# Performance work log

Measured on AMD Instinct MI355X. Metric: run time of the kernel, lower is better.

The kernel has to match this reference:

```python
import jax, jax.numpy as jnp
import numpy as np

V, H, L, T, B, S = 32000, 1024, 2, 64, 32, 64


def setup_inputs() -> dict:
    key = jax.random.key(0)
    ks = jax.random.split(key, 10)
    sc = 0.02
    return {
        "tokens": jax.random.randint(ks[0], (T, B), 0, V),
        "h0": jax.random.normal(ks[1], (L, B, H), jnp.float32) * sc,
        "c0": jax.random.normal(ks[2], (L, B, H), jnp.float32) * sc,
        "contexts": jax.random.normal(ks[3], (B, S, H), jnp.float32) * sc,
        "emb": jax.random.normal(ks[4], (V, H), jnp.float32) * sc,
        "W_ih": jax.random.normal(ks[5], (L, 4 * H, H), jnp.float32) * sc,
        "W_hh": jax.random.normal(ks[6], (L, 4 * H, H), jnp.float32) * sc,
        "b_ih": jnp.zeros((L, 4 * H), jnp.float32),
        "b_hh": jnp.zeros((L, 4 * H), jnp.float32),
        "W_in": jax.random.normal(ks[7], (H, H), jnp.float32) * sc,
        "b_in": jnp.zeros((H,), jnp.float32),
        "W_out": jax.random.normal(ks[8], (H, 2 * H), jnp.float32) * sc,
        "b_out": jnp.zeros((H,), jnp.float32),
    }


def _lstm_cell(x, h, c, Wih, Whh, bih, bhh):
    # PyTorch LSTMCell gate order: i, f, g, o
    gates = x @ Wih.T + bih + h @ Whh.T + bhh  # [B, 4H]
    i, f, g, o = jnp.split(gates, 4, axis=-1)
    c1 = jax.nn.sigmoid(f) * c + jax.nn.sigmoid(i) * jnp.tanh(g)
    h1 = jax.nn.sigmoid(o) * jnp.tanh(c1)
    return h1, c1


def reference(tokens, h0, c0, contexts, emb, W_ih, W_hh, b_ih, b_hh,
              W_in, b_in, W_out, b_out):
    # dropout is identity in eval mode
    embs = emb[tokens]  # [T, B, H]
    n_layers = h0.shape[0]

    def step(carry, x):
        h, c = carry
        hs, cs = [], []
        inp = x
        for l in range(n_layers):
            h1, c1 = _lstm_cell(inp, h[l], c[l], W_ih[l], W_hh[l], b_ih[l], b_hh[l])
            inp = h1
            hs.append(h1)
            cs.append(c1)
        # global (Luong general) attention
        gamma = inp @ W_in.T + b_in                      # [B, H]
        scores = jnp.einsum("bsh,bh->bs", contexts, gamma)
        w = jax.nn.softmax(scores, axis=-1)              # [B, S]
        ctx = jnp.einsum("bs,bsh->bh", w, contexts)      # [B, H]
        out = jnp.tanh(jnp.concatenate([ctx, inp], axis=-1) @ W_out.T + b_out)
        return (jnp.stack(hs), jnp.stack(cs)), (out, w)

    (hT, cT), (outputs, attns) = jax.lax.scan(step, (h0, c0), embs)
    return outputs, hT, cT  # outputs: [T, B, H]
```

## Files before the change

kernel.cpp:

```cpp
#include <hip/hip_runtime.h>
#include <hip/hip_bf16.h>

#define HDIM 1024
#define BDIM 32
#define TDIM 64
#define SDIM 64
#define NBLK 256

typedef __attribute__((ext_vector_type(8))) short short8;
typedef __attribute__((ext_vector_type(4))) short s4v;
typedef __attribute__((ext_vector_type(4))) float f32x4;
typedef unsigned short ushort;
typedef unsigned int uint;

__device__ __forceinline__ float sigm(float x){ return 1.f/(1.f+expf(-x)); }
__device__ __forceinline__ ushort f2bf(float x){
  uint u = __float_as_uint(x);
  u = (u + 0x7FFF + ((u>>16)&1)) >> 16;
  return (ushort)u;
}
#define MFMA16(a,b,c) __builtin_amdgcn_mfma_f32_16x16x32_bf16((a),(b),(c),0,0,0)
#define ALD(p)     __hip_atomic_load((p), __ATOMIC_RELAXED, __HIP_MEMORY_SCOPE_AGENT)
#define AST(p,v)   __hip_atomic_store((p),(v), __ATOMIC_RELAXED, __HIP_MEMORY_SCOPE_AGENT)


__global__ void init_state_kernel(const float* __restrict__ h0,
                                  ushort* __restrict__ h0h,
                                  ushort* __restrict__ h1h){
  int i = blockIdx.x*256 + threadIdx.x;
  int l = i >> 15, r = i & 32767;
  int b = r >> 10, h = r & 1023;
  ushort* dst = l ? h1h : h0h;
  dst[(h>>2)*128 + b*4 + (h&3)] = f2bf(h0[i]);
}

__global__ void bar_init_kernel(int* flags){
  for(int i=threadIdx.x; i<1024; i+=256) flags[i] = 0;
}

__global__ void cast_kernel(const float* __restrict__ src, ushort* __restrict__ dst, int n4){
  int i = blockIdx.x*256 + threadIdx.x;
  if(i < n4){
    float4 v = ((const float4*)src)[i];
    ushort4 o; o.x=f2bf(v.x); o.y=f2bf(v.y); o.z=f2bf(v.z); o.w=f2bf(v.w);
    ((ushort4*)dst)[i] = o;
  }
}

__global__ void transpose_ctx_kernel(const float* __restrict__ ctx, ushort* __restrict__ ctxT){
  int b = blockIdx.y;
  int n = blockIdx.x*64 + (threadIdx.x & 63);
  int s0 = (threadIdx.x >> 6) * 16;
  for(int s=s0; s<s0+16; s++){
    float v = ctx[((size_t)b*SDIM + s)*HDIM + n];
    ctxT[((size_t)b*HDIM + n)*SDIM + s] = f2bf(v);
  }
}

__global__ void bias_kernel(const float* __restrict__ b_ih, const float* __restrict__ b_hh,
                            float* __restrict__ bias0, float* __restrict__ bias1){
  int i = blockIdx.x*256 + threadIdx.x;
  bias0[i] = b_ih[i] + b_hh[i];
  bias1[i] = b_ih[4096+i] + b_hh[4096+i];
}

__global__ void embed_kernel(const int* __restrict__ tokens,
                             const float* __restrict__ emb,
                             ushort* __restrict__ Xb){
  int tb = blockIdx.x;
  int tok = tokens[tb];
  const float4* src = (const float4*)(emb + (size_t)tok*HDIM);
  ushort4* dst = (ushort4*)(Xb + (size_t)tb*HDIM);
  float4 v = src[threadIdx.x];
  ushort4 o; o.x=f2bf(v.x); o.y=f2bf(v.y); o.z=f2bf(v.z); o.w=f2bf(v.w);
  dst[threadIdx.x] = o;
}

__global__ __launch_bounds__(256) void gemm_mfma_bt(
    const ushort* __restrict__ A0, const ushort* __restrict__ A1, int lda, int KSPLIT,
    const ushort* __restrict__ B, int ldb,
    const float* __restrict__ bias,
    float* __restrict__ C, int ldc, int K, int act){
  __shared__ ushort As[64][40];
  __shared__ ushort Bs[64][40];
  const int bm = blockIdx.y*64, bn = blockIdx.x*64;
  const int tid = threadIdx.x, w = tid>>6, lane = tid&63;
  const int quad = lane>>4, l16 = lane&15;
  const int mh = (w>>1)*32, nh = (w&1)*32;
  const int arow = tid>>2, aseg = (tid&3)*8;
  f32x4 acc[2][2];
  #pragma unroll
  for(int i=0;i<2;i++)
    #pragma unroll
    for(int j=0;j<2;j++) acc[i][j] = (f32x4){0.f,0.f,0.f,0.f};

  for(int k0=0;k0<K;k0+=32){
    int gk = k0 + aseg;
    const ushort* ap = (gk < KSPLIT) ? (A0 + (size_t)(bm+arow)*lda + gk)
                                     : (A1 + (size_t)(bm+arow)*lda + (gk - KSPLIT));
    *(float4*)&As[arow][aseg] = *(const float4*)ap;
    *(float4*)&Bs[arow][aseg] = *(const float4*)(B + (size_t)(bn+arow)*ldb + k0 + aseg);
    __syncthreads();
    short8 a0 = *(const short8*)&As[mh + l16][quad*8];
    short8 a1 = *(const short8*)&As[mh + 16 + l16][quad*8];
    short8 b0 = *(const short8*)&Bs[nh + l16][quad*8];
    short8 b1 = *(const short8*)&Bs[nh + 16 + l16][quad*8];
    acc[0][0] = MFMA16(a0, b0, acc[0][0]);
    acc[0][1] = MFMA16(a0, b1, acc[0][1]);
    acc[1][0] = MFMA16(a1, b0, acc[1][0]);
    acc[1][1] = MFMA16(a1, b1, acc[1][1]);
    __syncthreads();
  }
  #pragma unroll
  for(int mi=0;mi<2;mi++){
    #pragma unroll
    for(int r=0;r<4;r++){
      int row = bm + mh + mi*16 + quad*4 + r;
      #pragma unroll
      for(int ni=0;ni<2;ni++){
        int col = bn + nh + ni*16 + l16;
        float v = acc[mi][ni][r];
        if(bias) v += bias[col];
        if(act==1) v = tanhf(v);
        if(act==2) ((ushort*)C)[(size_t)row*ldc + col] = f2bf(v);
        else       C[(size_t)row*ldc + col] = v;
      }
    }
  }
}

__global__ __launch_bounds__(256,1) void lstm_skew(
    const ushort* __restrict__ Whh0b,
    const ushort* __restrict__ Wih1b,
    const ushort* __restrict__ Whh1b,
    const float*  __restrict__ G0,
    const float*  __restrict__ bias1c,
    const float*  __restrict__ c0in,
    ushort* __restrict__ h0h,
    ushort* __restrict__ h1h,
    ushort* __restrict__ inp_bf,
    float*  __restrict__ outstate,
    int* __restrict__ flags){
  extern __shared__ char smem[];
  ushort (*W0s)[1032]   = (ushort(*)[1032])smem;
  ushort (*W1s)[2056]   = (ushort(*)[2056])(smem + 33024);
  float (*gred0)[32][17] = (float(*)[32][17])(smem + 98816);
  float (*gred1)[32][17] = (float(*)[32][17])(smem + 107520);
  float (*cloc0)[4]      = (float(*)[4])(smem + 116224);
  float (*cloc1)[4]      = (float(*)[4])(smem + 116736);

  const int tid = threadIdx.x, w = tid>>6, lane = tid&63;
  const int quad = lane>>4, l16 = lane&15;
  const int blk = blockIdx.x;
  const int j0 = blk*4;

  {
    int r = tid>>4, seg = tid&15;
    int wr = (r>>2)*1024 + j0 + (r&3);
    const ushort* s0 = Whh0b + (size_t)wr*1024 + seg*64;
    const ushort* s1 = Wih1b + (size_t)wr*1024 + seg*64;
    const ushort* s2 = Whh1b + (size_t)wr*1024 + seg*64;
    #pragma unroll
    for(int u=0; u<64; u+=8){
      *(short8*)&W0s[r][seg*64+u]       = *(const short8*)(s0+u);
      *(short8*)&W1s[r][seg*64+u]       = *(const short8*)(s1+u);
      *(short8*)&W1s[r][1024+seg*64+u]  = *(const short8*)(s2+u);
    }
  }
  if(tid < 128){
    int b = tid>>2, jj = tid&3;
    cloc0[b][jj] = c0in[b*1024 + j0 + jj];
    cloc1[b][jj] = c0in[32768 + b*1024 + j0 + jj];
  }
  float2 pbI={0,0}, pbF={0,0}, pbG={0,0}, pbO={0,0};
  if(tid >= 64 && tid < 128){
    const float* br = bias1c + j0 + ((tid-64)&1)*2;
    pbI = *(const float2*)(br);
    pbF = *(const float2*)(br+1024);
    pbG = *(const float2*)(br+2048);
    pbO = *(const float2*)(br+3072);
  }
  __syncthreads();

  for(int p=0; p<=TDIM; p++){
    const ushort* h0p = h0h + (size_t)p*32768;
    ushort*       h0n = h0h + (size_t)(p+1)*32768;
    const ushort* h1m = h1h + (size_t)(p>0?p-1:0)*32768;
    ushort*       h1c = h1h + (size_t)p*32768;
    float2 pgI={0,0}, pgF={0,0}, pgG={0,0}, pgO={0,0};
    if(p < TDIM && tid < 64){
      const float* g0r = G0 + (size_t)(p*32+(tid>>1))*4096 + j0 + (tid&1)*2;
      pgI = *(const float2*)(g0r);
      pgF = *(const float2*)(g0r+1024);
      pgG = *(const float2*)(g0r+2048);
      pgO = *(const float2*)(g0r+3072);
    }
    if(p < TDIM){
      f32x4 acc0 = {0,0,0,0}, acc1 = {0,0,0,0};
      const int kbase = w*256;
      #pragma unroll
      for(int kc=0;kc<8;kc++){
        int k0 = kbase + kc*32 + quad*8;
        const ushort* pa = h0p + (k0>>2)*128 + l16*4;
        s4v a0lo = *(const s4v*)pa;
        s4v a0hi = *(const s4v*)(pa + 128);
        s4v a1lo = *(const s4v*)(pa + 64);
        s4v a1hi = *(const s4v*)(pa + 192);
        short8 af0 = __builtin_shufflevector(a0lo, a0hi, 0,1,2,3,4,5,6,7);
        short8 af1 = __builtin_shufflevector(a1lo, a1hi, 0,1,2,3,4,5,6,7);
        short8 bfrag = *(const short8*)&W0s[l16][k0];
        acc0 = MFMA16(af0, bfrag, acc0);
        acc1 = MFMA16(af1, bfrag, acc1);
      }
      #pragma unroll
      for(int r=0;r<4;r++){
        gred0[w][quad*4+r][l16]    = acc0[r];
        gred0[w][16+quad*4+r][l16] = acc1[r];
      }
    }
    if(p > 0){
      f32x4 acc0 = {0,0,0,0}, acc1 = {0,0,0,0};
      const ushort* hb1 = (w < 2) ? h0p : h1m;
      const int kb = (w&1)*512;
      #pragma unroll
      for(int kc=0;kc<16;kc++){
        int k0 = kb + kc*32 + quad*8;
        const ushort* pa = hb1 + (k0>>2)*128 + l16*4;
        s4v a0lo = *(const s4v*)pa;
        s4v a0hi = *(const s4v*)(pa + 128);
        s4v a1lo = *(const s4v*)(pa + 64);
        s4v a1hi = *(const s4v*)(pa + 192);
        short8 af0 = __builtin_shufflevector(a0lo, a0hi, 0,1,2,3,4,5,6,7);
        short8 af1 = __builtin_shufflevector(a1lo, a1hi, 0,1,2,3,4,5,6,7);
        short8 bfrag = *(const short8*)&W1s[l16][w*512 + kc*32 + quad*8];
        acc0 = MFMA16(af0, bfrag, acc0);
        acc1 = MFMA16(af1, bfrag, acc1);
      }
      #pragma unroll
      for(int r=0;r<4;r++){
        gred1[w][quad*4+r][l16]    = acc0[r];
        gred1[w][16+quad*4+r][l16] = acc1[r];
      }
    }
    __syncthreads();
    if(p < TDIM && tid < 64){
      int b = tid>>1, j2 = (tid&1)*2;
      ushort hv[2];
      #pragma unroll
      for(int u=0;u<2;u++){
        int jj = j2+u;
        float gi = u ? pgI.y : pgI.x;
        float gf = u ? pgF.y : pgF.x;
        float gg = u ? pgG.y : pgG.x;
        float go = u ? pgO.y : pgO.x;
        #pragma unroll
        for(int ww=0;ww<4;ww++){
          gi += gred0[ww][b][jj];    gf += gred0[ww][b][4+jj];
          gg += gred0[ww][b][8+jj];  go += gred0[ww][b][12+jj];
        }
        float c = cloc0[b][jj];
        float c1 = sigm(gf)*c + sigm(gi)*tanhf(gg);
        float h1 = sigm(go)*tanhf(c1);
        cloc0[b][jj] = c1;
        hv[u] = f2bf(h1);
        if(p==TDIM-1){
          outstate[b*1024 + j0 + jj] = h1;
          outstate[65536 + b*1024 + j0 + jj] = c1;
        }
      }
      uint pk = (uint)hv[0] | ((uint)hv[1] << 16);
      AST((uint*)(h0n + blk*128 + b*4 + j2), pk);
    }
    if(p > 0 && tid >= 64 && tid < 128){
      int ct = tid-64;
      int b = ct>>1, j2 = (ct&1)*2;
      ushort hv[2];
      #pragma unroll
      for(int u=0;u<2;u++){
        int jj = j2+u;
        float gi = u ? pbI.y : pbI.x;
        float gf = u ? pbF.y : pbF.x;
        float gg = u ? pbG.y : pbG.x;
        float go = u ? pbO.y : pbO.x;
        #pragma unroll
        for(int ww=0;ww<4;ww++){
          gi += gred1[ww][b][jj];    gf += gred1[ww][b][4+jj];
          gg += gred1[ww][b][8+jj];  go += gred1[ww][b][12+jj];
        }
        float c = cloc1[b][jj];
        float c1 = sigm(gf)*c + sigm(gi)*tanhf(gg);
        float h1 = sigm(go)*tanhf(c1);
        cloc1[b][jj] = c1;
        hv[u] = f2bf(h1);
        inp_bf[(size_t)((p-1)*32+b)*1024 + j0 + jj] = hv[u];
        if(p==TDIM){
          outstate[32768 + b*1024 + j0 + jj] = h1;
          outstate[98304 + b*1024 + j0 + jj] = c1;
        }
      }
      uint pk = (uint)hv[0] | ((uint)hv[1] << 16);
      AST((uint*)(h1c + blk*128 + b*4 + j2), pk);
    }
    if(p == TDIM) break;
    __syncthreads();
    const int target = p+1;
    if(tid==0) AST(&flags[blk], target);
    if(blk==0 && tid<64){
      while(true){
        int v0 = ALD(&flags[tid]);
        int v1 = ALD(&flags[tid+64]);
        int v2 = ALD(&flags[tid+128]);
        int v3 = ALD(&flags[tid+192]);
        int mn = min(min(v0,v1),min(v2,v3));
        if(__all(mn >= target)) break;
        __builtin_amdgcn_s_sleep(2);
      }
      if(tid<16) AST(&flags[512 + tid*32], target);
    }
    if(tid==0){
      while(ALD(&flags[512 + (blk>>4)*32]) < target) __builtin_amdgcn_s_sleep(8);
    }
    __syncthreads();
  }
}

__global__ __launch_bounds__(256) void attn_mfma(
    const ushort* __restrict__ gamma_bf,
    const ushort* __restrict__ ctxb,
    const ushort* __restrict__ ctxT,
    ushort* __restrict__ ctx_out){
  const int b = blockIdx.y, t0 = blockIdx.x*16;
  const int tid = threadIdx.x, w = tid>>6, lane = tid&63;
  const int quad = lane>>4, l16 = lane&15;
  __shared__ float S[16][68];
  __shared__ ushort Pb[16][72];
  {
    f32x4 acc = {0,0,0,0};
    const ushort* arow = gamma_bf + ((size_t)(t0+l16)*32 + b)*1024;
    const ushort* brow = ctxb + ((size_t)b*SDIM + w*16 + l16)*1024;
    #pragma unroll 8
    for(int kc=0;kc<32;kc++){
      short8 af = *(const short8*)(arow + kc*32 + quad*8);
      short8 bf = *(const short8*)(brow + kc*32 + quad*8);
      acc = MFMA16(af, bf, acc);
    }
    #pragma unroll
    for(int r=0;r<4;r++) S[quad*4+r][w*16+l16] = acc[r];
  }
  __syncthreads();
  if(tid < 16){
    float mx = -1e30f;
    for(int s=0;s<SDIM;s++) mx = fmaxf(mx, S[tid][s]);
    float sum = 0.f;
    for(int s=0;s<SDIM;s++) sum += expf(S[tid][s]-mx);
    float inv = 1.f/sum;
    for(int s=0;s<SDIM;s++) Pb[tid][s] = f2bf(expf(S[tid][s]-mx)*inv);
  }
  __syncthreads();
  const ushort* bbase = ctxT + ((size_t)b*HDIM + w*256)*SDIM;
  for(int nt=0; nt<16; nt++){
    f32x4 acc = {0,0,0,0};
    #pragma unroll
    for(int kc=0;kc<2;kc++){
      short8 af = *(const short8*)&Pb[l16][kc*32 + quad*8];
      short8 bf = *(const short8*)(bbase + (size_t)(nt*16+l16)*SDIM + kc*32 + quad*8);
      acc = MFMA16(af, bf, acc);
    }
    int n = w*256 + nt*16 + l16;
    #pragma unroll
    for(int r=0;r<4;r++){
      int t = t0 + quad*4 + r;
      ctx_out[((size_t)t*32 + b)*1024 + n] = f2bf(acc[r]);
    }
  }
}

extern "C" void kernel_launch(void* const* d_in, const int* in_sizes, int n_in,
                              void* d_out, int out_size, void* d_ws, size_t ws_size,
                              hipStream_t stream){
  const int*   tokens   = (const int*)  d_in[0];
  const float* h0       = (const float*)d_in[1];
  const float* c0       = (const float*)d_in[2];
  const float* contexts = (const float*)d_in[3];
  const float* emb      = (const float*)d_in[4];
  const float* W_ih     = (const float*)d_in[5];
  const float* W_hh     = (const float*)d_in[6];
  const float* b_ih     = (const float*)d_in[7];
  const float* b_hh     = (const float*)d_in[8];
  const float* W_in     = (const float*)d_in[9];
  const float* b_in     = (const float*)d_in[10];
  const float* W_out    = (const float*)d_in[11];
  const float* b_out    = (const float*)d_in[12];

  float* out = (float*)d_out;
  const int TB = TDIM*BDIM;

  char* wp = (char*)d_ws;
  float* G0      = (float*)wp;  wp += (size_t)TB*4*HDIM*4;
  float* bias0c  = (float*)wp;  wp += 4096*4;
  float* bias1c  = (float*)wp;  wp += 4096*4;
  int*   flags   = (int*)wp;    wp += 4096;
  ushort* X_bf   = (ushort*)wp; wp += (size_t)TB*HDIM*2;
  ushort* Wih0b  = (ushort*)wp; wp += (size_t)4*HDIM*HDIM*2;
  ushort* Whh0b  = (ushort*)wp; wp += (size_t)4*HDIM*HDIM*2;
  ushort* Wih1b  = (ushort*)wp; wp += (size_t)4*HDIM*HDIM*2;
  ushort* Whh1b  = (ushort*)wp; wp += (size_t)4*HDIM*HDIM*2;
  ushort* Winb   = (ushort*)wp; wp += (size_t)HDIM*HDIM*2;
  ushort* Woutb  = (ushort*)wp; wp += (size_t)HDIM*2*HDIM*2;
  ushort* inp_bf = (ushort*)wp; wp += (size_t)TB*HDIM*2;
  ushort* h0hist = (ushort*)wp; wp += (size_t)(TDIM+1)*BDIM*HDIM*2;
  ushort* h1hist = (ushort*)wp; wp += (size_t)(TDIM+1)*BDIM*HDIM*2;
  ushort* ctxb_bf= (ushort*)wp; wp += (size_t)BDIM*SDIM*HDIM*2;
  ushort* ctxT_bf= (ushort*)wp; wp += (size_t)BDIM*SDIM*HDIM*2;
  ushort* gammaB = (ushort*)G0;
  ushort* ctx_bf = X_bf;

  init_state_kernel<<<256,256,0,stream>>>(h0, h0hist, h1hist);
  bar_init_kernel<<<1,256,0,stream>>>(flags);
  cast_kernel<<<4096,256,0,stream>>>(W_ih,                       Wih0b, 4*HDIM*HDIM/4);
  cast_kernel<<<4096,256,0,stream>>>(W_hh,                       Whh0b, 4*HDIM*HDIM/4);
  cast_kernel<<<4096,256,0,stream>>>(W_ih + (size_t)4*HDIM*HDIM, Wih1b, 4*HDIM*HDIM/4);
  cast_kernel<<<4096,256,0,stream>>>(W_hh + (size_t)4*HDIM*HDIM, Whh1b, 4*HDIM*HDIM/4);
  cast_kernel<<<1024,256,0,stream>>>(W_in,  Winb,  HDIM*HDIM/4);
  cast_kernel<<<2048,256,0,stream>>>(W_out, Woutb, HDIM*2*HDIM/4);
  cast_kernel<<<2048,256,0,stream>>>(contexts, ctxb_bf, BDIM*SDIM*HDIM/4);
  transpose_ctx_kernel<<<dim3(16,32),256,0,stream>>>(contexts, ctxT_bf);
  bias_kernel<<<16,256,0,stream>>>(b_ih, b_hh, bias0c, bias1c);
  embed_kernel<<<TB,256,0,stream>>>(tokens, emb, X_bf);

  gemm_mfma_bt<<<dim3(4*HDIM/64, TB/64),256,0,stream>>>(
      X_bf, X_bf, HDIM, HDIM, Wih0b, HDIM, bias0c, G0, 4*HDIM, HDIM, 0);

  lstm_skew<<<NBLK,256,117248,stream>>>(
      Whh0b, Wih1b, Whh1b, G0, bias1c, c0,
      h0hist, h1hist, inp_bf, out + (size_t)TB*HDIM, flags);

  gemm_mfma_bt<<<dim3(HDIM/64, TB/64),256,0,stream>>>(
      inp_bf, inp_bf, HDIM, HDIM, Winb, HDIM, b_in, (float*)gammaB, HDIM, HDIM, 2);

  attn_mfma<<<dim3(4,32),256,0,stream>>>(gammaB, ctxb_bf, ctxT_bf, ctx_bf);

  gemm_mfma_bt<<<dim3(HDIM/64, TB/64),256,0,stream>>>(
      ctx_bf, inp_bf, HDIM, HDIM, Woutb, 2*HDIM, b_out, out, HDIM, 2*HDIM, 1);
}
```

Measured before the change: 930.2 us.

## Batch hidden-state loads upfront and slim grid barrier with double-buffered reductions

Issues all hidden-state fragment loads for both layers up front with inline-asm dwordx2 loads and one waitcnt, so the loads no longer sit between MFMAs. Double-buffers the gred reduction buffers by step parity, which removes the pre-barrier __syncthreads. The grid barrier now has per-wave flags written by the two writer waves after their stores drain, and every thread polls the release flag, which drops the trailing __syncthreads. This adds register pressure (96 s4v per thread) and a larger LDS footprint, and it relies on memory ordering held by relaxed atomics plus waitcnt.

```diff
diff --git a/kernel.cpp b/kernel.cpp
--- a/kernel.cpp
+++ b/kernel.cpp
@@ -22,6 +22,21 @@
 #define MFMA16(a,b,c) __builtin_amdgcn_mfma_f32_16x16x32_bf16((a),(b),(c),0,0,0)
 #define ALD(p)     __hip_atomic_load((p), __ATOMIC_RELAXED, __HIP_MEMORY_SCOPE_AGENT)
 #define AST(p,v)   __hip_atomic_store((p),(v), __ATOMIC_RELAXED, __HIP_MEMORY_SCOPE_AGENT)
+
+__device__ __forceinline__ void load8(const char* b, s4v* r){
+  asm volatile(
+    "global_load_dwordx2 %0, %8, off\n\t"
+    "global_load_dwordx2 %1, %8, off offset:128\n\t"
+    "global_load_dwordx2 %2, %8, off offset:256\n\t"
+    "global_load_dwordx2 %3, %8, off offset:384\n\t"
+    "global_load_dwordx2 %4, %8, off offset:2048\n\t"
+    "global_load_dwordx2 %5, %8, off offset:2176\n\t"
+    "global_load_dwordx2 %6, %8, off offset:2304\n\t"
+    "global_load_dwordx2 %7, %8, off offset:2432\n\t"
+    : "=&v"(r[0]), "=&v"(r[1]), "=&v"(r[2]), "=&v"(r[3]),
+      "=&v"(r[4]), "=&v"(r[5]), "=&v"(r[6]), "=&v"(r[7])
+    : "v"(b) : "memory");
+}
 
 
 __global__ void init_state_kernel(const float* __restrict__ h0,
@@ -144,10 +159,11 @@
   extern __shared__ char smem[];
   ushort (*W0s)[1032]   = (ushort(*)[1032])smem;
   ushort (*W1s)[2056]   = (ushort(*)[2056])(smem + 33024);
-  float (*gred0)[32][17] = (float(*)[32][17])(smem + 98816);
-  float (*gred1)[32][17] = (float(*)[32][17])(smem + 107520);
-  float (*cloc0)[4]      = (float(*)[4])(smem + 116224);
-  float (*cloc1)[4]      = (float(*)[4])(smem + 116736);
+  typedef float gredT[4][32][17];
+  gredT* gred0 = (gredT*)(smem + 98816);
+  gredT* gred1 = (gredT*)(smem + 116224);
+  float (*cloc0)[4]      = (float(*)[4])(smem + 133632);
+  float (*cloc1)[4]      = (float(*)[4])(smem + 134144);
 
   const int tid = threadIdx.x, w = tid>>6, lane = tid&63;
   const int quad = lane>>4, l16 = lane&15;
@@ -183,10 +199,12 @@
   __syncthreads();
 
   for(int p=0; p<=TDIM; p++){
+    const int par = p&1;
     const ushort* h0p = h0h + (size_t)p*32768;
     ushort*       h0n = h0h + (size_t)(p+1)*32768;
     const ushort* h1m = h1h + (size_t)(p>0?p-1:0)*32768;
     ushort*       h1c = h1h + (size_t)p*32768;
+
     float2 pgI={0,0}, pgF={0,0}, pgG={0,0}, pgO={0,0};
     if(p < TDIM && tid < 64){
       const float* g0r = G0 + (size_t)(p*32+(tid>>1))*4096 + j0 + (tid&1)*2;
@@ -195,51 +213,53 @@
       pgG = *(const float2*)(g0r+2048);
       pgO = *(const float2*)(g0r+3072);
     }
+
+    s4v r0[32]; s4v r1[64];
+    if(p < TDIM){
+      const char* b0 = (const char*)h0p + w*16384 + quad*512 + l16*8;
+      load8(b0,        r0);
+      load8(b0+4096,   r0+8);
+      load8(b0+8192,   r0+16);
+      load8(b0+12288,  r0+24);
+    }
+    if(p > 0){
+      const char* b1 = (const char*)((w<2)?h0p:h1m) + (w&1)*32768 + quad*512 + l16*8;
+      #pragma unroll
+      for(int i=0;i<8;i++) load8(b1 + i*4096, r1 + i*8);
+    }
+    asm volatile("s_waitcnt vmcnt(0)" ::: "memory");
+    __builtin_amdgcn_sched_barrier(0);
+
     if(p < TDIM){
       f32x4 acc0 = {0,0,0,0}, acc1 = {0,0,0,0};
-      const int kbase = w*256;
       #pragma unroll
       for(int kc=0;kc<8;kc++){
-        int k0 = kbase + kc*32 + quad*8;
-        const ushort* pa = h0p + (k0>>2)*128 + l16*4;
-        s4v a0lo = *(const s4v*)pa;
-        s4v a0hi = *(const s4v*)(pa + 128);
-        s4v a1lo = *(const s4v*)(pa + 64);
-        s4v a1hi = *(const s4v*)(pa + 192);
-        short8 af0 = __builtin_shufflevector(a0lo, a0hi, 0,1,2,3,4,5,6,7);
-        short8 af1 = __builtin_shufflevector(a1lo, a1hi, 0,1,2,3,4,5,6,7);
-        short8 bfrag = *(const short8*)&W0s[l16][k0];
+        short8 af0 = __builtin_shufflevector(r0[kc*4+0], r0[kc*4+2], 0,1,2,3,4,5,6,7);
+        short8 af1 = __builtin_shufflevector(r0[kc*4+1], r0[kc*4+3], 0,1,2,3,4,5,6,7);
+        short8 bfrag = *(const short8*)&W0s[l16][w*256 + kc*32 + quad*8];
         acc0 = MFMA16(af0, bfrag, acc0);
         acc1 = MFMA16(af1, bfrag, acc1);
       }
       #pragma unroll
       for(int r=0;r<4;r++){
-        gred0[w][quad*4+r][l16]    = acc0[r];
-        gred0[w][16+quad*4+r][l16] = acc1[r];
+        gred0[par][w][quad*4+r][l16]    = acc0[r];
+        gred0[par][w][16+quad*4+r][l16] = acc1[r];
       }
     }
     if(p > 0){
       f32x4 acc0 = {0,0,0,0}, acc1 = {0,0,0,0};
-      const ushort* hb1 = (w < 2) ? h0p : h1m;
-      const int kb = (w&1)*512;
       #pragma unroll
       for(int kc=0;kc<16;kc++){
-        int k0 = kb + kc*32 + quad*8;
-        const ushort* pa = hb1 + (k0>>2)*128 + l16*4;
-        s4v a0lo = *(const s4v*)pa;
-        s4v a0hi = *(const s4v*)(pa + 128);
-        s4v a1lo = *(const s4v*)(pa + 64);
-        s4v a1hi = *(const s4v*)(pa + 192);
-        short8 af0 = __builtin_shufflevector(a0lo, a0hi, 0,1,2,3,4,5,6,7);
-        short8 af1 = __builtin_shufflevector(a1lo, a1hi, 0,1,2,3,4,5,6,7);
+        short8 af0 = __builtin_shufflevector(r1[kc*4+0], r1[kc*4+2], 0,1,2,3,4,5,6,7);
+        short8 af1 = __builtin_shufflevector(r1[kc*4+1], r1[kc*4+3], 0,1,2,3,4,5,6,7);
         short8 bfrag = *(const short8*)&W1s[l16][w*512 + kc*32 + quad*8];
         acc0 = MFMA16(af0, bfrag, acc0);
         acc1 = MFMA16(af1, bfrag, acc1);
       }
       #pragma unroll
       for(int r=0;r<4;r++){
-        gred1[w][quad*4+r][l16]    = acc0[r];
-        gred1[w][16+quad*4+r][l16] = acc1[r];
+        gred1[par][w][quad*4+r][l16]    = acc0[r];
+        gred1[par][w][16+quad*4+r][l16] = acc1[r];
       }
     }
     __syncthreads();
@@ -255,8 +275,8 @@
         float go = u ? pgO.y : pgO.x;
         #pragma unroll
         for(int ww=0;ww<4;ww++){
-          gi += gred0[ww][b][jj];    gf += gred0[ww][b][4+jj];
-          gg += gred0[ww][b][8+jj];  go += gred0[ww][b][12+jj];
+          gi += gred0[par][ww][b][jj];    gf += gred0[par][ww][b][4+jj];
+          gg += gred0[par][ww][b][8+jj];  go += gred0[par][ww][b][12+jj];
         }
         float c = cloc0[b][jj];
         float c1 = sigm(gf)*c + sigm(gi)*tanhf(gg);
@@ -284,8 +304,8 @@
         float go = u ? pbO.y : pbO.x;
         #pragma unroll
         for(int ww=0;ww<4;ww++){
-          gi += gred1[ww][b][jj];    gf += gred1[ww][b][4+jj];
-          gg += gred1[ww][b][8+jj];  go += gred1[ww][b][12+jj];
+          gi += gred1[par][ww][b][jj];    gf += gred1[par][ww][b][4+jj];
+          gg += gred1[par][ww][b][8+jj];  go += gred1[par][ww][b][12+jj];
         }
         float c = cloc1[b][jj];
         float c1 = sigm(gf)*c + sigm(gi)*tanhf(gg);
@@ -302,25 +322,23 @@
       AST((uint*)(h1c + blk*128 + b*4 + j2), pk);
     }
     if(p == TDIM) break;
-    __syncthreads();
+
     const int target = p+1;
-    if(tid==0) AST(&flags[blk], target);
-    if(blk==0 && tid<64){
+    if(tid < 128){
+      asm volatile("s_waitcnt vmcnt(0)" ::: "memory");
+      if((tid&63)==0) AST(&flags[blk*2 + w], target);
+    }
+    if(blk==0 && tid < 64){
       while(true){
-        int v0 = ALD(&flags[tid]);
-        int v1 = ALD(&flags[tid+64]);
-        int v2 = ALD(&flags[tid+128]);
-        int v3 = ALD(&flags[tid+192]);
-        int mn = min(min(v0,v1),min(v2,v3));
+        int mn = 0x7fffffff;
+        #pragma unroll
+        for(int q=0;q<8;q++){ int v = ALD(&flags[tid + q*64]); mn = min(mn, v); }
         if(__all(mn >= target)) break;
-        __builtin_amdgcn_s_sleep(2);
-      }
-      if(tid<16) AST(&flags[512 + tid*32], target);
-    }
-    if(tid==0){
-      while(ALD(&flags[512 + (blk>>4)*32]) < target) __builtin_amdgcn_s_sleep(8);
-    }
-    __syncthreads();
+        __builtin_amdgcn_s_sleep(1);
+      }
+      if(tid < 16) AST(&flags[512 + tid*32], target);
+    }
+    while(ALD(&flags[512 + (blk>>4)*32]) < target) __builtin_amdgcn_s_sleep(1);
   }
 }
 
@@ -431,7 +449,7 @@
   gemm_mfma_bt<<<dim3(4*HDIM/64, TB/64),256,0,stream>>>(
       X_bf, X_bf, HDIM, HDIM, Wih0b, HDIM, bias0c, G0, 4*HDIM, HDIM, 0);
 
-  lstm_skew<<<NBLK,256,117248,stream>>>(
+  lstm_skew<<<NBLK,256,134656,stream>>>(
       Whh0b, Wih1b, Whh1b, G0, bias1c, c0,
       h0hist, h1hist, inp_bf, out + (size_t)TB*HDIM, flags);
 
```

Result: faster. 890.4 us (-4.3%).
